# Performance work log

Measured on AMD Instinct MI355X. Metric: run time of the kernel, lower is better.

The kernel has to match this reference:

```python
import jax, jax.numpy as jnp
import numpy as np

BN_EPS = 1e-5

def setup_inputs() -> dict:
    key = jax.random.key(0)
    ks = jax.random.split(key, 10)
    B, Cin, Cout, H, W = 4, 256, 128, 64, 64
    Cqk = Cout // 8  # 16
    return {
        "x": jax.random.normal(ks[0], (B, Cin, H, W), dtype=jnp.float32),
        "conv_w": jax.random.normal(ks[1], (Cout, Cin, 3, 3), dtype=jnp.float32) * 0.03,
        "bn_gamma": jnp.ones((Cout,), dtype=jnp.float32),
        "bn_beta": jnp.zeros((Cout,), dtype=jnp.float32),
        "q_w": jax.random.normal(ks[2], (Cqk, Cout), dtype=jnp.float32) * 0.05,
        "q_b": jnp.zeros((Cqk,), dtype=jnp.float32),
        "k_w": jax.random.normal(ks[3], (Cqk, Cout), dtype=jnp.float32) * 0.05,
        "k_b": jnp.zeros((Cqk,), dtype=jnp.float32),
        "v_w": jax.random.normal(ks[4], (Cout, Cout), dtype=jnp.float32) * 0.05,
        "v_b": jnp.zeros((Cout,), dtype=jnp.float32),
        # gamma params are zero-init in the original; use small nonzero values so the
        # attention branches actually contribute (better correctness signal).
        "gamma_ca": jax.random.normal(ks[5], (1,), dtype=jnp.float32) * 0.1,
        "gamma_pa": jax.random.normal(ks[6], (1,), dtype=jnp.float32) * 0.1,
    }

def _conv_bn_relu(x, conv_w, bn_gamma, bn_beta):
    # 3x3 conv, stride 1, pad 1, no bias (NCHW / OIHW)
    y = jax.lax.conv_general_dilated(
        x, conv_w, window_strides=(1, 1), padding=((1, 1), (1, 1)),
        dimension_numbers=("NCHW", "OIHW", "NCHW"))
    # BatchNorm2d in training mode: batch statistics over (N, H, W)
    mean = jnp.mean(y, axis=(0, 2, 3), keepdims=True)
    var = jnp.var(y, axis=(0, 2, 3), keepdims=True)
    y = (y - mean) * jax.lax.rsqrt(var + BN_EPS)
    y = y * bn_gamma[None, :, None, None] + bn_beta[None, :, None, None]
    return jax.nn.relu(y)

def _cam(feat, gamma):
    B, C, H, W = feat.shape
    f = feat.reshape(B, C, H * W)                       # (B, C, N)
    energy = jnp.einsum("bcn,bdn->bcd", f, f)           # (B, C, C)
    energy_new = jnp.max(energy, axis=-1, keepdims=True) - energy
    attn = jnp.tanh(energy_new)
    out = jnp.einsum("bcd,bdn->bcn", attn, f).reshape(B, C, H, W)
    return gamma * out + feat

def _pam(feat, q_w, q_b, k_w, k_b, v_w, v_b, gamma):
    B, C, H, W = feat.shape
    N = H * W
    f = feat.reshape(B, C, N)
    q = jnp.einsum("oc,bcn->bon", q_w, f) + q_b[None, :, None]   # (B, C//8, N)
    k = jnp.einsum("oc,bcn->bon", k_w, f) + k_b[None, :, None]
    v = jnp.einsum("oc,bcn->bon", v_w, f) + v_b[None, :, None]   # (B, C, N)
    energy = jnp.einsum("bqn,bqm->bnm", q, k)                    # (B, N, N)
    attn = jnp.tanh(energy)
    # torch: bmm(value, attention^T): out[b,c,m] = sum_n v[b,c,n] * attn[b,m,n]
    out = jnp.einsum("bcn,bmn->bcm", v, attn).reshape(B, C, H, W)
    return gamma * out + feat

def reference(x, conv_w, bn_gamma, bn_beta, q_w, q_b, k_w, k_b, v_w, v_b, gamma_ca, gamma_pa):
    feat = _conv_bn_relu(x, conv_w, bn_gamma, bn_beta)
    out_ca = _cam(feat, gamma_ca)
    out_sa = _pam(feat, q_w, q_b, k_w, k_b, v_w, v_b, gamma_pa)
    return out_ca + out_sa + feat
```

## Files before the change

### kernel.cpp

```cpp
#include <hip/hip_runtime.h>
#include <math.h>

#define BATCH 4
#define CIN   256
#define CCH   128
#define HW    4096
#define CQK   16

using short8   = __attribute__((ext_vector_type(8))) short;
using floatx4  = __attribute__((ext_vector_type(4))) float;
using floatx16 = __attribute__((ext_vector_type(16))) float;
using uint4v   = __attribute__((ext_vector_type(4))) unsigned int;

__device__ __forceinline__ float fast_tanh(float x) {
    float e = __builtin_amdgcn_exp2f(x * 2.8853900817779268f);
    float r = __builtin_amdgcn_rcpf(e + 1.0f);
    return __builtin_fmaf(-2.0f, r, 1.0f);
}

__device__ __forceinline__ unsigned short f2bf(float f) {
    unsigned u = __float_as_uint(f);
    u += 0x7fff + ((u >> 16) & 1);
    return (unsigned short)(u >> 16);
}

__device__ __forceinline__ float bf2f(unsigned short u) {
    return __uint_as_float(((unsigned)u) << 16);
}

#define ROWMAP(r, hi) (((r) & 3) + (((r) >> 2) << 3) + ((hi) << 2))

#define XTP_ROW   (66 * 256)
#define XTP_BATCH (66 * 66 * 256)

__global__ __launch_bounds__(256) void prep_all_kernel(
        const float* __restrict__ x, const float* __restrict__ w,
        const float* __restrict__ qw, const float* __restrict__ qb,
        const float* __restrict__ kw, const float* __restrict__ kb,
        const float* __restrict__ vw, const float* __restrict__ vb,
        unsigned short* __restrict__ xTp, unsigned short* __restrict__ Wb2,
        unsigned short* __restrict__ Wqkv, float* __restrict__ biasAll,
        float* __restrict__ statsS, float* __restrict__ statsQ) {
    const int bx = blockIdx.x, tid = threadIdx.x;
    if (bx < 1024) {
        __shared__ unsigned short lds[64][72];
        const int ci0 = (bx & 3) << 6, yr = (bx >> 2) & 63, b = bx >> 8;
        const int cir = tid >> 2, xc = tid & 3;
        const float* xp = x + (((b << 8) + ci0 + cir) << 12) + (yr << 6) + xc * 16;
#pragma unroll
        for (int j = 0; j < 4; ++j) {
            float4 v = *(const float4*)(xp + j * 4);
            int xi = xc * 16 + j * 4;
            lds[xi + 0][cir] = f2bf(v.x);
            lds[xi + 1][cir] = f2bf(v.y);
            lds[xi + 2][cir] = f2bf(v.z);
            lds[xi + 3][cir] = f2bf(v.w);
        }
        const short8 z8 = (short8){0,0,0,0,0,0,0,0};
        if (tid < 16) {
            int col = (tid >> 3) ? 65 : 0;
            int part = tid & 7;
            *(short8*)(xTp + b * XTP_BATCH + (yr + 1) * XTP_ROW + col * 256 +
                       ci0 + part * 8) = z8;
        }
        if (yr == 0 || yr == 63) {
            int row = (yr == 0) ? 0 : 65;
            for (int e = tid; e < 528; e += 256) {
                int xi = e >> 3, part = e & 7;
                *(short8*)(xTp + b * XTP_BATCH + row * XTP_ROW + xi * 256 +
                           ci0 + part * 8) = z8;
            }
        }
        __syncthreads();
        const int xr = tid >> 2, part = tid & 3;
        unsigned short* dst = xTp + b * XTP_BATCH + (yr + 1) * XTP_ROW +
                              (xr + 1) * 256 + ci0 + part * 16;
        *(short8*)(dst + 0) = *(const short8*)&lds[xr][part * 16 + 0];
        *(short8*)(dst + 8) = *(const short8*)&lds[xr][part * 16 + 8];
    } else if (bx < 2176) {
        int o = (bx - 1024) * 256 + tid;
        int s   = o & 31;
        int co  = (o >> 5) & 127;
        int cc  = (o >> 12) & 7;
        int tap = o >> 15;
        int ci  = (cc << 5) + s;
        Wb2[o] = f2bf(w[co * 2304 + ci * 9 + tap]);
    } else if (bx < 2256) {
        int idx = (bx - 2176) * 256 + tid;
        int o = idx >> 7, c = idx & 127;
        float wv = (o < 16) ? qw[(o << 7) + c]
                 : (o < 32) ? kw[((o - 16) << 7) + c]
                            : vw[((o - 32) << 7) + c];
        Wqkv[idx] = f2bf(wv);
        if (idx < 160)
            biasAll[idx] = (idx < 16) ? qb[idx] : (idx < 32) ? kb[idx - 16] : vb[idx - 32];
    } else {
        if (tid < 128) { statsS[tid] = 0.f; statsQ[tid] = 0.f; }
    }
}

#define LOADBAND(R, KY)                                                        \
    {                                                                          \
        const unsigned short* g_ = bandbase + (KY) * XTP_ROW;                  \
        _Pragma("unroll")                                                      \
        for (int j = 0; j < 4; ++j)                                            \
            R[j] = *(const short8*)(g_ + ((tid + j * 256) << 3));              \
        if (tid < 64) R[4] = *(const short8*)(g_ + ((1024 + tid) << 3));       \
    }

#define WRITEBAND(R, BUF)                                                      \
    {                                                                          \
        char* p_ = (char*)&Bl[BUF][0];                                         \
        _Pragma("unroll")                                                      \
        for (int j = 0; j < 4; ++j) {                                          \
            int bb_ = (tid + j * 256) << 4;                                    \
            *(short8*)(p_ + (bb_ ^ (((bb_ >> 9) & 7) << 4))) = R[j];           \
        }                                                                      \
        if (tid < 64) {                                                        \
            int bb_ = (1024 + tid) << 4;                                       \
            *(short8*)(p_ + (bb_ ^ (((bb_ >> 9) & 7) << 4))) = R[4];           \
        }                                                                      \
    }

#define LOADA(P, TAP)                                                          \
    {                                                                          \
        const unsigned short* ar_ = Wb2 + ((TAP) << 15) + (aco0 << 5) + (quad << 3); \
        _Pragma("unroll")                                                      \
        for (int cc = 0; cc < 8; ++cc) {                                       \
            P[2 * cc]     = *(const short8*)(ar_ + (cc << 12));                \
            P[2 * cc + 1] = *(const short8*)(ar_ + (cc << 12) + 512);          \
        }                                                                      \
    }

#define CONVSTEP(BUF, KX, PC, PN, TAPN, PREF)                                  \
    {                                                                          \
        const char* bp_ = (const char*)&Bl[BUF][0];                            \
        const int pl0_ = l15 + (KX);                                           \
        const int sw_ = (pl0_ & 7) << 4;                                       \
        const int b0_ = (pl0_ << 9) + (quad << 4);                             \
        const int b1_ = b0_ + (16 << 9);                                       \
        const unsigned short* arn_ = Wb2 + ((TAPN) << 15) + (aco0 << 5) + (quad << 3); \
        _Pragma("unroll")                                                      \
        for (int cc = 0; cc < 8; ++cc) {                                       \
            if (PREF) {                                                        \
                PN[2 * cc]     = *(const short8*)(arn_ + (cc << 12));          \
                PN[2 * cc + 1] = *(const short8*)(arn_ + (cc << 12) + 512);    \
            }                                                                  \
            short8 bf0 = *(const short8*)(bp_ + ((b0_ + (cc << 6)) ^ sw_));    \
            short8 bf1 = *(const short8*)(bp_ + ((b1_ + (cc << 6)) ^ sw_));    \
            acc00 = __builtin_amdgcn_mfma_f32_16x16x32_bf16(PC[2 * cc], bf0, acc00, 0, 0, 0); \
            acc01 = __builtin_amdgcn_mfma_f32_16x16x32_bf16(PC[2 * cc], bf1, acc01, 0, 0, 0); \
            acc10 = __builtin_amdgcn_mfma_f32_16x16x32_bf16(PC[2 * cc + 1], bf0, acc10, 0, 0, 0); \
            acc11 = __builtin_amdgcn_mfma_f32_16x16x32_bf16(PC[2 * cc + 1], bf1, acc11, 0, 0, 0); \
        }                                                                      \
    }

__global__ __launch_bounds__(256, 2) void conv_mfma_kernel(
        const unsigned short* __restrict__ xTp, const unsigned short* __restrict__ Wb2,
        float* __restrict__ y, float* __restrict__ convP) {
    const int tid = threadIdx.x;
    const int w = tid >> 6, lane = tid & 63, l15 = lane & 15, quad = lane >> 4;
    const int idx = blockIdx.x;
    const int xcd = idx & 7, rr = idx >> 3;
    const int yl = rr & 7, ph = (rr >> 3) & 1, b = rr >> 4;
    const int yr = (xcd << 3) + yl;
    const int cobase = w << 5;
    const int px0 = ph << 5;
    const int aco0 = cobase + l15;

    __shared__ __align__(16) unsigned short Bl[2][8704];

    const unsigned short* bandbase = xTp + b * XTP_BATCH + yr * XTP_ROW + (px0 << 8);

    floatx4 acc00 = (floatx4){0.f, 0.f, 0.f, 0.f};
    floatx4 acc01 = (floatx4){0.f, 0.f, 0.f, 0.f};
    floatx4 acc10 = (floatx4){0.f, 0.f, 0.f, 0.f};
    floatx4 acc11 = (floatx4){0.f, 0.f, 0.f, 0.f};

    short8 r0[5], r1[5], r2[5];
    short8 AbA[16], AbB[16];

    LOADBAND(r0, 0);
    WRITEBAND(r0, 0);
    LOADBAND(r1, 1);
    LOADA(AbA, 0);
    __syncthreads();

    WRITEBAND(r1, 1);
    LOADBAND(r2, 2);
    CONVSTEP(0, 0, AbA, AbB, 1, 1)
    CONVSTEP(0, 1, AbB, AbA, 2, 1)
    CONVSTEP(0, 2, AbA, AbB, 3, 1)
    __syncthreads();

    WRITEBAND(r2, 0);
    CONVSTEP(1, 0, AbB, AbA, 4, 1)
    CONVSTEP(1, 1, AbA, AbB, 5, 1)
    CONVSTEP(1, 2, AbB, AbA, 6, 1)
    __syncthreads();

    CONVSTEP(0, 0, AbA, AbB, 7, 1)
    CONVSTEP(0, 1, AbB, AbA, 8, 1)
    CONVSTEP(0, 2, AbA, AbB, 0, 0)

#pragma unroll
    for (int ns = 0; ns < 2; ++ns) {
        int px = px0 + (ns << 4) + l15;
        floatx4 a0 = ns ? acc01 : acc00;
        floatx4 a1 = ns ? acc11 : acc10;
#pragma unroll
        for (int r = 0; r < 4; ++r) {
            int co0 = cobase + (quad << 2) + r;
            y[(((b << 7) + co0) << 12) + (yr << 6) + px] = a0[r];
            y[(((b << 7) + co0 + 16) << 12) + (yr << 6) + px] = a1[r];
        }
    }

#pragma unroll
    for (int ms = 0; ms < 2; ++ms) {
        floatx4 aa = ms ? acc10 : acc00;
        floatx4 ab = ms ? acc11 : acc01;
#pragma unroll
        for (int r = 0; r < 4; ++r) {
            float s = aa[r] + ab[r];
            float q = aa[r] * aa[r] + ab[r] * ab[r];
#pragma unroll
            for (int off = 1; off < 16; off <<= 1) {
                s += __shfl_xor(s, off);
                q += __shfl_xor(q, off);
            }
            if (l15 == 0) {
                int co = cobase + ms * 16 + (quad << 2) + r;
                convP[(co << 9) + idx] = s;
                convP[((128 + co) << 9) + idx] = q;
            }
        }
    }
}

__global__ __launch_bounds__(64) void stats_reduce_kernel(
        const float* __restrict__ convP, float* __restrict__ statsS,
        float* __restrict__ statsQ) {
    const int s = blockIdx.x, t = threadIdx.x;
    const float* p = convP + (s << 9);
    float v = 0.f;
#pragma unroll
    for (int j = 0; j < 8; ++j) v += p[t + (j << 6)];
#pragma unroll
    for (int off = 32; off; off >>= 1) v += __shfl_xor(v, off);
    if (t == 0) {
        if (s < 128) statsS[s] = v;
        else         statsQ[s - 128] = v;
    }
}

__global__ __launch_bounds__(256) void bn_apply_kernel(
        const float* __restrict__ y, const float* __restrict__ statsS,
        const float* __restrict__ statsQ, const float* __restrict__ gamma,
        const float* __restrict__ beta, unsigned short* __restrict__ featB,
        unsigned short* __restrict__ fT) {
    __shared__ unsigned short lds[64][72];
    const int tid = threadIdx.x;
    const int c0 = blockIdx.x * 64, n0 = blockIdx.y * 64, b = blockIdx.z;
    const int cir = tid >> 2, xc = tid & 3;
    const int c = c0 + cir;
    const float S = statsS[c], Q = statsQ[c];
    const float mean = S * (1.f / 16384.f);
    const float var  = Q * (1.f / 16384.f) - mean * mean;
    const float rstd = rsqrtf(var + 1e-5f);
    const float sc = gamma[c] * rstd;
    const float sh = beta[c] - mean * sc;
    const float* yp = y + (((b << 7) + c) << 12) + n0 + xc * 16;
    unsigned short* fp = featB + (((b << 7) + c) << 12) + n0 + xc * 16;
#pragma unroll
    for (int j = 0; j < 4; ++j) {
        float4 v = *(const float4*)(yp + j * 4);
        ushort4 o;
        o.x = f2bf(fmaxf(fmaf(v.x, sc, sh), 0.f));
        o.y = f2bf(fmaxf(fmaf(v.y, sc, sh), 0.f));
        o.z = f2bf(fmaxf(fmaf(v.z, sc, sh), 0.f));
        o.w = f2bf(fmaxf(fmaf(v.w, sc, sh), 0.f));
        *(ushort4*)(fp + j * 4) = o;
        int ni = xc * 16 + j * 4;
        lds[ni + 0][cir] = o.x;
        lds[ni + 1][cir] = o.y;
        lds[ni + 2][cir] = o.z;
        lds[ni + 3][cir] = o.w;
    }
    __syncthreads();
    const int nr = tid >> 2, part = tid & 3;
    unsigned short* dst = fT + (((b << 12) + n0 + nr) << 7) + c0 + part * 16;
    *(short8*)(dst + 0) = *(const short8*)&lds[nr][part * 16 + 0];
    *(short8*)(dst + 8) = *(const short8*)&lds[nr][part * 16 + 8];
}

__global__ __launch_bounds__(256) void camqkv_kernel(
        const unsigned short* __restrict__ featB, float* __restrict__ ep,
        const unsigned short* __restrict__ Wqkv, const float* __restrict__ biasAll,
        const unsigned short* __restrict__ fT,
        unsigned short* __restrict__ qT, unsigned short* __restrict__ kT,
        unsigned short* __restrict__ vB) {
    const int bx = blockIdx.x, tid = threadIdx.x;
    const int l31 = tid & 31, hi = (tid >> 5) & 1;
    if (bx < 256) {
        const int kc = bx & 63, b = bx >> 6, wv = tid >> 6;
        floatx16 acc[4];
#pragma unroll
        for (int t = 0; t < 4; ++t)
#pragma unroll
            for (int r = 0; r < 16; ++r) acc[t][r] = 0.f;
        for (int s = 0; s < 4; ++s) {
            const int k0 = (kc << 6) + (s << 4) + (hi << 3);
            short8 fr = *(const short8*)&featB[(((b << 7) + (wv << 5) + l31) << 12) + k0];
            short8 fc0 = *(const short8*)&featB[(((b << 7) +  0 + l31) << 12) + k0];
            short8 fc1 = *(const short8*)&featB[(((b << 7) + 32 + l31) << 12) + k0];
            short8 fc2 = *(const short8*)&featB[(((b << 7) + 64 + l31) << 12) + k0];
            short8 fc3 = *(const short8*)&featB[(((b << 7) + 96 + l31) << 12) + k0];
            acc[0] = __builtin_amdgcn_mfma_f32_32x32x16_bf16(fr, fc0, acc[0], 0, 0, 0);
            acc[1] = __builtin_amdgcn_mfma_f32_32x32x16_bf16(fr, fc1, acc[1], 0, 0, 0);
            acc[2] = __builtin_amdgcn_mfma_f32_32x32x16_bf16(fr, fc2, acc[2], 0, 0, 0);
            acc[3] = __builtin_amdgcn_mfma_f32_32x32x16_bf16(fr, fc3, acc[3], 0, 0, 0);
        }
#pragma unroll
        for (int t = 0; t < 4; ++t)
#pragma unroll
            for (int r = 0; r < 16; ++r) {
                int c = ((tid >> 6) << 5) + ROWMAP(r, hi);
                int d = (t << 5) + l31;
                ep[(((kc << 2) + b) << 14) + (c << 7) + d] = acc[t][r];
            }
    } else {
        const int bi = bx - 256, b = bi >> 6, w = tid >> 6;
        const int n0 = ((bi & 63) << 6) + ((w >> 1) << 5);
        const int tstart = (w & 1) ? 3 : 0;
        const int tcnt   = (w & 1) ? 2 : 3;
        floatx16 acc[3];
#pragma unroll
        for (int t = 0; t < 3; ++t)
#pragma unroll
            for (int r = 0; r < 16; ++r) acc[t][r] = 0.f;
        for (int s = 0; s < 8; ++s) {
            const int k0 = (s << 4) + (hi << 3);
            short8 bf = *(const short8*)&fT[(((b << 12) + n0 + l31) << 7) + k0];
#pragma unroll
            for (int ti = 0; ti < 3; ++ti) {
                if (ti < tcnt) {
                    short8 aw = *(const short8*)&Wqkv[((((tstart + ti) << 5) + l31) << 7) + k0];
                    acc[ti] = __builtin_amdgcn_mfma_f32_32x32x16_bf16(aw, bf, acc[ti], 0, 0, 0);
                }
            }
        }
        const int n = n0 + l31;
#pragma unroll
        for (int ti = 0; ti < 3; ++ti) {
            if (ti >= tcnt) continue;
            const int t = tstart + ti;
#pragma unroll
            for (int r = 0; r < 16; ++r) {
                int o = (t << 5) + ROWMAP(r, hi);
                float val = acc[ti][r] + biasAll[o];
                if (t == 0) {
                    if (o < 16) qT[(((b << 12) + n) << 4) + o] = f2bf(val);
                    else        kT[(((b << 12) + n) << 4) + o - 16] = f2bf(val);
                } else if (o >= 32) {
                    vB[(((b << 7) + o - 32) << 12) + n] = f2bf(val);
                }
            }
        }
    }
}

#define PAM_STEP(LB, NC)                                                          \
    {                                                                             \
        const unsigned short* lb_ = (LB);                                         \
        const int na_ = nbase + ((NC) << 5);                                      \
        short8 avl0 = *(const short8*)(lb_ + ( l31       * 40) + hi * 8);         \
        short8 avh0 = *(const short8*)(lb_ + ( l31       * 40) + 16 + hi * 8);    \
        short8 avl1 = *(const short8*)(lb_ + ((32 + l31) * 40) + hi * 8);         \
        short8 avh1 = *(const short8*)(lb_ + ((32 + l31) * 40) + 16 + hi * 8);    \
        short8 avl2 = *(const short8*)(lb_ + ((64 + l31) * 40) + hi * 8);         \
        short8 avh2 = *(const short8*)(lb_ + ((64 + l31) * 40) + 16 + hi * 8);    \
        short8 avl3 = *(const short8*)(lb_ + ((96 + l31) * 40) + hi * 8);         \
        short8 avh3 = *(const short8*)(lb_ + ((96 + l31) * 40) + 16 + hi * 8);    \
        floatx16 s_ = __builtin_amdgcn_mfma_f32_32x32x16_bf16(ak, bq, zero16, 0, 0, 0); \
        if ((NC) < 31)                                                            \
            ak = *(const short8*)&kT[(((b << 12) + na_ + 32 + l31) << 4) + hi * 8]; \
        unsigned p_[8];                                                           \
        _Pragma("unroll")                                                         \
        for (int i = 0; i < 8; ++i) {                                             \
            float t0 = fast_tanh(s_[2 * i]);                                      \
            float t1 = fast_tanh(s_[2 * i + 1]);                                  \
            p_[i] = (__float_as_uint(t1) & 0xFFFF0000u) | (__float_as_uint(t0) >> 16); \
        }                                                                         \
        unsigned sh_[8];                                                          \
        _Pragma("unroll")                                                         \
        for (int i = 0; i < 8; ++i) sh_[i] = __shfl_xor(p_[i], 32, 64);           \
        uint4v b1u, b2u;                                                          \
        b1u[0] = hi ? sh_[2] : p_[0];                                             \
        b1u[1] = hi ? sh_[3] : p_[1];                                             \
        b1u[2] = hi ? p_[2] : sh_[0];                                             \
        b1u[3] = hi ? p_[3] : sh_[1];                                             \
        b2u[0] = hi ? sh_[6] : p_[4];                                             \
        b2u[1] = hi ? sh_[7] : p_[5];                                             \
        b2u[2] = hi ? p_[6] : sh_[4];                                             \
        b2u[3] = hi ? p_[7] : sh_[5];                                             \
        short8 B1 = __builtin_bit_cast(short8, b1u);                              \
        short8 B2 = __builtin_bit_cast(short8, b2u);                              \
        __builtin_amdgcn_s_setprio(1);                                            \
        acc[0] = __builtin_amdgcn_mfma_f32_32x32x16_bf16(avl0, B1, acc[0], 0, 0, 0); \
        acc[0] = __builtin_amdgcn_mfma_f32_32x32x16_bf16(avh0, B2, acc[0], 0, 0, 0); \
        acc[1] = __builtin_amdgcn_mfma_f32_32x32x16_bf16(avl1, B1, acc[1], 0, 0, 0); \
        acc[1] = __builtin_amdgcn_mfma_f32_32x32x16_bf16(avh1, B2, acc[1], 0, 0, 0); \
        acc[2] = __builtin_amdgcn_mfma_f32_32x32x16_bf16(avl2, B1, acc[2], 0, 0, 0); \
        acc[2] = __builtin_amdgcn_mfma_f32_32x32x16_bf16(avh2, B2, acc[2], 0, 0, 0); \
        acc[3] = __builtin_amdgcn_mfma_f32_32x32x16_bf16(avl3, B1, acc[3], 0, 0, 0); \
        acc[3] = __builtin_amdgcn_mfma_f32_32x32x16_bf16(avh3, B2, acc[3], 0, 0, 0); \
        __builtin_amdgcn_s_setprio(0);                                            \
    }

__global__ __launch_bounds__(256) void pam_attn_kernel(
        const unsigned short* __restrict__ qT, const unsigned short* __restrict__ kT,
        const unsigned short* __restrict__ vB, unsigned short* __restrict__ pamP,
        const float* __restrict__ ep, unsigned short* __restrict__ attnB) {
    const int bx = blockIdx.x, tid = threadIdx.x;
    if (bx < 512) {
        const int nh = bx & 3, b = bx >> 7;
        const int w = tid >> 6, lane = tid & 63, l31 = lane & 31, hi = lane >> 5;
        const int m0 = (((bx >> 2) & 31) << 7) + (w << 5);

        __shared__ __align__(16) unsigned short vtile[2][5120];

        short8 bq = *(const short8*)&qT[(((b << 12) + m0 + l31) << 4) + hi * 8];

        floatx16 acc[4], zero16;
#pragma unroll
        for (int r = 0; r < 16; ++r) {
            acc[0][r] = 0.f; acc[1][r] = 0.f; acc[2][r] = 0.f; acc[3][r] = 0.f;
            zero16[r] = 0.f;
        }

        const int nbase = nh << 10;

        const int srow = tid >> 1, shalf = tid & 1;
        const unsigned short* vg = vB + (((b << 7) + srow) << 12) + nbase + shalf * 16;
        unsigned short* sw0 = &vtile[0][srow * 40 + shalf * 16];
        unsigned short* sw1 = &vtile[1][srow * 40 + shalf * 16];

        short8 ak = *(const short8*)&kT[(((b << 12) + nbase + l31) << 4) + hi * 8];

        short8 gA0 = *(const short8*)(vg + 0);
        short8 gA1 = *(const short8*)(vg + 8);
        short8 gB0 = *(const short8*)(vg + 32);
        short8 gB1 = *(const short8*)(vg + 40);
        *(short8*)(sw0 + 0) = gA0;
        *(short8*)(sw0 + 8) = gA1;

        for (int t = 0; t < 16; ++t) {
            const int e = t << 1;
            __syncthreads();
            *(short8*)(sw1 + 0) = gB0;
            *(short8*)(sw1 + 8) = gB1;
            if (t < 15) {
                gA0 = *(const short8*)(vg + (e + 2) * 32);
                gA1 = *(const short8*)(vg + (e + 2) * 32 + 8);
            }
            PAM_STEP(&vtile[0][0], e);
            __syncthreads();
            if (t < 15) {
                *(short8*)(sw0 + 0) = gA0;
                *(short8*)(sw0 + 8) = gA1;
                gB0 = *(const short8*)(vg + (e + 3) * 32);
                gB1 = *(const short8*)(vg + (e + 3) * 32 + 8);
            }
            PAM_STEP(&vtile[1][0], e + 1);
        }

        const int pbase = (((nh << 2) + b) << 19) + m0 + l31;
#pragma unroll
        for (int ct = 0; ct < 4; ++ct)
#pragma unroll
            for (int r = 0; r < 16; ++r) {
                int c = (ct << 5) + ROWMAP(r, hi);
                pamP[pbase + (c << 12)] = f2bf(acc[ct][r]);
            }
    } else {
        const int bi = bx - 512, b = bi >> 6;
        const int half = tid >> 7, t = tid & 127;
        const int c = ((bi & 63) << 1) + half;
        float v = 0.f;
#pragma unroll 8
        for (int s = 0; s < 64; ++s)
            v += ep[(((s << 2) + b) << 14) + (c << 7) + t];
        float m = v;
        for (int off = 32; off; off >>= 1) m = fmaxf(m, __shfl_down(m, off));
        __shared__ float mx[4];
        if ((tid & 63) == 0) mx[tid >> 6] = m;
        __syncthreads();
        float M = fmaxf(mx[half << 1], mx[(half << 1) + 1]);
        attnB[(b << 14) + (c << 7) + t] = f2bf(fast_tanh(M - v));
    }
}

__global__ __launch_bounds__(256) void combine_kernel(
        const unsigned short* __restrict__ attnB, const unsigned short* __restrict__ fT,
        const unsigned short* __restrict__ featB, const unsigned short* __restrict__ pamP,
        const float* __restrict__ gca, const float* __restrict__ gpa,
        float* __restrict__ out) {
    const int b = blockIdx.y, tid = threadIdx.x;
    const int w = tid >> 6, l31 = tid & 31, hi = (tid >> 5) & 1;
    const int m0 = (blockIdx.x << 6) + ((w >> 1) << 5);
    const int ct0 = (w & 1) << 1;
    floatx16 acc[2];
#pragma unroll
    for (int t = 0; t < 2; ++t)
#pragma unroll
        for (int r = 0; r < 16; ++r) acc[t][r] = 0.f;

    for (int s = 0; s < 8; ++s) {
        const int k0 = (s << 4) + (hi << 3);
        short8 bf = *(const short8*)&fT[(((b << 12) + m0 + l31) << 7) + k0];
        short8 a0 = *(const short8*)&attnB[(b << 14) + ((((ct0 + 0) << 5) + l31) << 7) + k0];
        short8 a1 = *(const short8*)&attnB[(b << 14) + ((((ct0 + 1) << 5) + l31) << 7) + k0];
        acc[0] = __builtin_amdgcn_mfma_f32_32x32x16_bf16(a0, bf, acc[0], 0, 0, 0);
        acc[1] = __builtin_amdgcn_mfma_f32_32x32x16_bf16(a1, bf, acc[1], 0, 0, 0);
    }
    const float gc = gca[0], gp = gpa[0];
    const int m = m0 + l31;
#pragma unroll
    for (int t = 0; t < 2; ++t)
#pragma unroll
        for (int r = 0; r < 16; ++r) {
            int c = ((ct0 + t) << 5) + ROWMAP(r, hi);
            int ci = (c << 12) + m;
            float p = bf2f(pamP[((0 * 4 + b) << 19) + ci]) +
                      bf2f(pamP[((1 * 4 + b) << 19) + ci]) +
                      bf2f(pamP[((2 * 4 + b) << 19) + ci]) +
                      bf2f(pamP[((3 * 4 + b) << 19) + ci]);
            float fb = bf2f(featB[(((b << 7) + c) << 12) + m]);
            out[(((b << 7) + c) << 12) + m] = 3.f * fb + gc * acc[t][r] + gp * p;
        }
}

extern "C" void kernel_launch(void* const* d_in, const int* in_sizes, int n_in,
                              void* d_out, int out_size, void* d_ws, size_t ws_size,
                              hipStream_t stream) {
    const float* x      = (const float*)d_in[0];
    const float* conv_w = (const float*)d_in[1];
    const float* bn_g   = (const float*)d_in[2];
    const float* bn_b   = (const float*)d_in[3];
    const float* q_w    = (const float*)d_in[4];
    const float* q_b    = (const float*)d_in[5];
    const float* k_w    = (const float*)d_in[6];
    const float* k_b    = (const float*)d_in[7];
    const float* v_w    = (const float*)d_in[8];
    const float* v_b    = (const float*)d_in[9];
    const float* gca    = (const float*)d_in[10];
    const float* gpa    = (const float*)d_in[11];
    float* out = (float*)d_out;

    float* ws = (float*)d_ws;
    float* convY  = ws;
    unsigned short* xTp = (unsigned short*)(ws + 2097152);
    float* ep     = ws + 4327424;
    unsigned short* Wb2  = (unsigned short*)(ws + 8521728);
    unsigned short* Wqkv = (unsigned short*)(ws + 8669184);
    float* statsS  = ws + 8679424;
    float* statsQ  = ws + 8679552;
    float* biasAll = ws + 8679680;
    unsigned short* attnB = (unsigned short*)(ws + 8679872);
    unsigned short* qT    = (unsigned short*)(ws + 8712640);
    unsigned short* kT    = (unsigned short*)(ws + 8843712);
    unsigned short* vB    = (unsigned short*)(ws + 8974784);
    unsigned short* featB = (unsigned short*)(ws + 10023360);
    unsigned short* fT    = (unsigned short*)(ws + 11071936);
    unsigned short* pamP  = (unsigned short*)ws;
    float* convP = ws + 4327424;

    prep_all_kernel<<<2257, 256, 0, stream>>>(x, conv_w, q_w, q_b, k_w, k_b,
                                              v_w, v_b, xTp, Wb2, Wqkv, biasAll,
                                              statsS, statsQ);
    conv_mfma_kernel<<<512, 256, 0, stream>>>(xTp, Wb2, convY, convP);
    stats_reduce_kernel<<<256, 64, 0, stream>>>(convP, statsS, statsQ);
    bn_apply_kernel<<<dim3(2, 64, 4), 256, 0, stream>>>(convY, statsS, statsQ,
                                                        bn_g, bn_b, featB, fT);
    camqkv_kernel<<<512, 256, 0, stream>>>(featB, ep, Wqkv, biasAll, fT, qT, kT, vB);
    pam_attn_kernel<<<768, 256, 0, stream>>>(qT, kT, vB, pamP, ep, attnB);
    combine_kernel<<<dim3(64, 4), 256, 0, stream>>>(attnB, fT, featB, pamP, gca, gpa, out);
}
```

Measured before the change: 175.9 us.

## Double V tile width in PAM attention, halve barriers, split LDS loads around MFMAs

```diff
diff --git a/kernel.cpp b/kernel.cpp
--- a/kernel.cpp
+++ b/kernel.cpp
@@ -370,21 +370,16 @@
     }
 }
 
-#define PAM_STEP(LB, NC)                                                          \
+#define PAM_SUB(LB, NC, S32)                                                      \
     {                                                                             \
         const unsigned short* lb_ = (LB);                                         \
-        const int na_ = nbase + ((NC) << 5);                                      \
-        short8 avl0 = *(const short8*)(lb_ + ( l31       * 40) + hi * 8);         \
-        short8 avh0 = *(const short8*)(lb_ + ( l31       * 40) + 16 + hi * 8);    \
-        short8 avl1 = *(const short8*)(lb_ + ((32 + l31) * 40) + hi * 8);         \
-        short8 avh1 = *(const short8*)(lb_ + ((32 + l31) * 40) + 16 + hi * 8);    \
-        short8 avl2 = *(const short8*)(lb_ + ((64 + l31) * 40) + hi * 8);         \
-        short8 avh2 = *(const short8*)(lb_ + ((64 + l31) * 40) + 16 + hi * 8);    \
-        short8 avl3 = *(const short8*)(lb_ + ((96 + l31) * 40) + hi * 8);         \
-        short8 avh3 = *(const short8*)(lb_ + ((96 + l31) * 40) + 16 + hi * 8);    \
         floatx16 s_ = __builtin_amdgcn_mfma_f32_32x32x16_bf16(ak, bq, zero16, 0, 0, 0); \
         if ((NC) < 31)                                                            \
-            ak = *(const short8*)&kT[(((b << 12) + na_ + 32 + l31) << 4) + hi * 8]; \
+            ak = *(const short8*)&kT[(((b << 12) + nbase + (((NC) + 1) << 5) + l31) << 4) + hi * 8]; \
+        short8 avl0 = *(const short8*)(lb_ + ( l31       * 68) + (S32) + hi * 8);         \
+        short8 avh0 = *(const short8*)(lb_ + ( l31       * 68) + (S32) + 16 + hi * 8);    \
+        short8 avl1 = *(const short8*)(lb_ + ((32 + l31) * 68) + (S32) + hi * 8);         \
+        short8 avh1 = *(const short8*)(lb_ + ((32 + l31) * 68) + (S32) + 16 + hi * 8);    \
         unsigned p_[8];                                                           \
         _Pragma("unroll")                                                         \
         for (int i = 0; i < 8; ++i) {                                             \
@@ -411,6 +406,12 @@
         acc[0] = __builtin_amdgcn_mfma_f32_32x32x16_bf16(avh0, B2, acc[0], 0, 0, 0); \
         acc[1] = __builtin_amdgcn_mfma_f32_32x32x16_bf16(avl1, B1, acc[1], 0, 0, 0); \
         acc[1] = __builtin_amdgcn_mfma_f32_32x32x16_bf16(avh1, B2, acc[1], 0, 0, 0); \
+        __builtin_amdgcn_s_setprio(0);                                            \
+        short8 avl2 = *(const short8*)(lb_ + ((64 + l31) * 68) + (S32) + hi * 8);         \
+        short8 avh2 = *(const short8*)(lb_ + ((64 + l31) * 68) + (S32) + 16 + hi * 8);    \
+        short8 avl3 = *(const short8*)(lb_ + ((96 + l31) * 68) + (S32) + hi * 8);         \
+        short8 avh3 = *(const short8*)(lb_ + ((96 + l31) * 68) + (S32) + 16 + hi * 8);    \
+        __builtin_amdgcn_s_setprio(1);                                            \
         acc[2] = __builtin_amdgcn_mfma_f32_32x32x16_bf16(avl2, B1, acc[2], 0, 0, 0); \
         acc[2] = __builtin_amdgcn_mfma_f32_32x32x16_bf16(avh2, B2, acc[2], 0, 0, 0); \
         acc[3] = __builtin_amdgcn_mfma_f32_32x32x16_bf16(avl3, B1, acc[3], 0, 0, 0); \
@@ -424,11 +425,11 @@
         const float* __restrict__ ep, unsigned short* __restrict__ attnB) {
     const int bx = blockIdx.x, tid = threadIdx.x;
     if (bx < 512) {
-        const int nh = bx & 3, b = bx >> 7;
+        const int nh = bx & 3, mtile = (bx >> 2) & 31, b = bx >> 7;
         const int w = tid >> 6, lane = tid & 63, l31 = lane & 31, hi = lane >> 5;
-        const int m0 = (((bx >> 2) & 31) << 7) + (w << 5);
-
-        __shared__ __align__(16) unsigned short vtile[2][5120];
+        const int m0 = (mtile << 7) + (w << 5);
+
+        __shared__ __align__(16) unsigned short vtile[2][8704];
 
         short8 bq = *(const short8*)&qT[(((b << 12) + m0 + l31) << 4) + hi * 8];
 
@@ -442,37 +443,54 @@
         const int nbase = nh << 10;
 
         const int srow = tid >> 1, shalf = tid & 1;
-        const unsigned short* vg = vB + (((b << 7) + srow) << 12) + nbase + shalf * 16;
-        unsigned short* sw0 = &vtile[0][srow * 40 + shalf * 16];
-        unsigned short* sw1 = &vtile[1][srow * 40 + shalf * 16];
+        const unsigned short* vg = vB + (((b << 7) + srow) << 12) + nbase + shalf * 32;
+        unsigned short* sw0 = &vtile[0][srow * 68 + shalf * 32];
+        unsigned short* sw1 = &vtile[1][srow * 68 + shalf * 32];
 
         short8 ak = *(const short8*)&kT[(((b << 12) + nbase + l31) << 4) + hi * 8];
 
         short8 gA0 = *(const short8*)(vg + 0);
         short8 gA1 = *(const short8*)(vg + 8);
-        short8 gB0 = *(const short8*)(vg + 32);
-        short8 gB1 = *(const short8*)(vg + 40);
-        *(short8*)(sw0 + 0) = gA0;
-        *(short8*)(sw0 + 8) = gA1;
-
-        for (int t = 0; t < 16; ++t) {
-            const int e = t << 1;
+        short8 gA2 = *(const short8*)(vg + 16);
+        short8 gA3 = *(const short8*)(vg + 24);
+        short8 gB0 = *(const short8*)(vg + 64);
+        short8 gB1 = *(const short8*)(vg + 72);
+        short8 gB2 = *(const short8*)(vg + 80);
+        short8 gB3 = *(const short8*)(vg + 88);
+        *(short8*)(sw0 + 0)  = gA0;
+        *(short8*)(sw0 + 8)  = gA1;
+        *(short8*)(sw0 + 16) = gA2;
+        *(short8*)(sw0 + 24) = gA3;
+
+        for (int t = 0; t < 8; ++t) {
             __syncthreads();
-            *(short8*)(sw1 + 0) = gB0;
-            *(short8*)(sw1 + 8) = gB1;
-            if (t < 15) {
-                gA0 = *(const short8*)(vg + (e + 2) * 32);
-                gA1 = *(const short8*)(vg + (e + 2) * 32 + 8);
-            }
-            PAM_STEP(&vtile[0][0], e);
+            *(short8*)(sw1 + 0)  = gB0;
+            *(short8*)(sw1 + 8)  = gB1;
+            *(short8*)(sw1 + 16) = gB2;
+            *(short8*)(sw1 + 24) = gB3;
+            if (t < 7) {
+                const unsigned short* s_ = vg + (2 * t + 2) * 64;
+                gA0 = *(const short8*)(s_ + 0);
+                gA1 = *(const short8*)(s_ + 8);
+                gA2 = *(const short8*)(s_ + 16);
+                gA3 = *(const short8*)(s_ + 24);
+            }
+            PAM_SUB(&vtile[0][0], 4 * t + 0, 0);
+            PAM_SUB(&vtile[0][0], 4 * t + 1, 32);
             __syncthreads();
-            if (t < 15) {
-                *(short8*)(sw0 + 0) = gA0;
-                *(short8*)(sw0 + 8) = gA1;
-                gB0 = *(const short8*)(vg + (e + 3) * 32);
-                gB1 = *(const short8*)(vg + (e + 3) * 32 + 8);
-            }
-            PAM_STEP(&vtile[1][0], e + 1);
+            if (t < 7) {
+                *(short8*)(sw0 + 0)  = gA0;
+                *(short8*)(sw0 + 8)  = gA1;
+                *(short8*)(sw0 + 16) = gA2;
+                *(short8*)(sw0 + 24) = gA3;
+                const unsigned short* s_ = vg + (2 * t + 3) * 64;
+                gB0 = *(const short8*)(s_ + 0);
+                gB1 = *(const short8*)(s_ + 8);
+                gB2 = *(const short8*)(s_ + 16);
+                gB3 = *(const short8*)(s_ + 24);
+            }
+            PAM_SUB(&vtile[1][0], 4 * t + 2, 0);
+            PAM_SUB(&vtile[1][0], 4 * t + 3, 32);
         }
 
         const int pbase = (((nh << 2) + b) << 19) + m0 + l31;
@@ -573,8 +591,8 @@
     unsigned short* vB    = (unsigned short*)(ws + 8974784);
     unsigned short* featB = (unsigned short*)(ws + 10023360);
     unsigned short* fT    = (unsigned short*)(ws + 11071936);
-    unsigned short* pamP  = (unsigned short*)ws;
     float* convP = ws + 4327424;
+    unsigned short* pamP = (unsigned short*)(ws + 12120512);
 
     prep_all_kernel<<<2257, 256, 0, stream>>>(x, conv_w, q_w, q_b, k_w, k_b,
                                               v_w, v_b, xTp, Wb2, Wqkv, biasAll,
```

Result: slower. 219.9 us (+25.0%).
